# Kernel tuning notes

Measured on AMD Instinct MI355X. Metric: run time of the kernel, lower is better.

The kernel has to match this reference:

```python
import jax, jax.numpy as jnp
import numpy as np

C = 512
N_HEADS = 8
K_CH = C // N_HEADS          # 64
ROPE_D = int(K_CH * 0.5)     # 32, only first half of head dim is rotated
ROPE_BASE = 10000


def apply_rope(x):
    # x: [b, h, t, k_ch]; rotate first ROPE_D features, pass the rest through.
    t = x.shape[2]
    d = ROPE_D
    theta = 1.0 / (ROPE_BASE ** (jnp.arange(0, d, 2, dtype=jnp.float32) / d))  # [d/2]
    idx_theta = jnp.arange(t, dtype=jnp.float32)[:, None] * theta[None, :]     # [t, d/2]
    angles = jnp.concatenate([idx_theta, idx_theta], axis=-1)                  # [t, d]
    cos = jnp.cos(angles)[None, None, :, :].astype(x.dtype)
    sin = jnp.sin(angles)[None, None, :, :].astype(x.dtype)
    x_rope, x_pass = x[..., :d], x[..., d:]
    d2 = d // 2
    neg_half = jnp.concatenate([-x_rope[..., d2:], x_rope[..., :d2]], axis=-1)
    x_rope = x_rope * cos + neg_half * sin
    return jnp.concatenate([x_rope, x_pass], axis=-1)


def setup_inputs() -> dict:
    key = jax.random.key(0)
    ks = jax.random.split(key, 9)
    B, T = 16, 1024
    scale = 1.0 / np.sqrt(C)
    return {
        "x": jax.random.normal(ks[0], (B, C, T), dtype=jnp.float32),
        "Wq": jax.random.normal(ks[1], (C, C), dtype=jnp.float32) * scale,
        "bq": jax.random.normal(ks[2], (C,), dtype=jnp.float32) * 0.01,
        "Wk": jax.random.normal(ks[3], (C, C), dtype=jnp.float32) * scale,
        "bk": jax.random.normal(ks[4], (C,), dtype=jnp.float32) * 0.01,
        "Wv": jax.random.normal(ks[5], (C, C), dtype=jnp.float32) * scale,
        "bv": jax.random.normal(ks[6], (C,), dtype=jnp.float32) * 0.01,
        "Wo": jax.random.normal(ks[7], (C, C), dtype=jnp.float32) * scale,
        "bo": jax.random.normal(ks[8], (C,), dtype=jnp.float32) * 0.01,
    }


def reference(x, Wq, bq, Wk, bk, Wv, bv, Wo, bo):
    b, c, t = x.shape
    # 1x1 conv == channel matmul: [o,c] x [b,c,t] -> [b,o,t]
    q = jnp.einsum('oc,bct->bot', Wq, x) + bq[None, :, None]
    k = jnp.einsum('oc,bct->bot', Wk, x) + bk[None, :, None]
    v = jnp.einsum('oc,bct->bot', Wv, x) + bv[None, :, None]

    def to_heads(z):  # [b, c, t] -> [b, h, t, k_ch]
        return z.reshape(b, N_HEADS, K_CH, t).transpose(0, 1, 3, 2)

    q = apply_rope(to_heads(q))
    k = apply_rope(to_heads(k))
    v = to_heads(v)

    # scaled dot product attention (scale = 1/sqrt(head_dim))
    scores = jnp.einsum('bhqd,bhkd->bhqk', q, k) / np.sqrt(K_CH).astype(np.float32)
    attn = jax.nn.softmax(scores, axis=-1)
    out = jnp.einsum('bhqk,bhkd->bhqd', attn, v)  # [b, h, t, k_ch]

    out = out.transpose(0, 1, 3, 2).reshape(b, c, t)  # [b, c, t]
    return jnp.einsum('oc,bct->bot', Wo, out) + bo[None, :, None]
```

## Files before the change

### kernel.cpp

```cpp
#include <hip/hip_runtime.h>
#include <cmath>

#define B_  16
#define T_  1024
#define C_  512
#define NH_ 8
#define HD_ 64

#define AS1 __attribute__((address_space(1)))
#define AS3 __attribute__((address_space(3)))

#define FENCE_VM()   asm volatile("s_waitcnt vmcnt(0)" ::: "memory")
#define FENCE_LGKM() asm volatile("s_waitcnt lgkmcnt(0)" ::: "memory")

typedef __bf16 bf16_t;
typedef __bf16 bf16x8 __attribute__((ext_vector_type(8)));
typedef __bf16 bf16x4 __attribute__((ext_vector_type(4)));
typedef short  shortx8 __attribute__((ext_vector_type(8)));
typedef short  shortx4 __attribute__((ext_vector_type(4)));
typedef float  floatx4 __attribute__((ext_vector_type(4)));
typedef float  float4v __attribute__((ext_vector_type(4)));

__device__ inline float fast_exp2(float x) {
#if __has_builtin(__builtin_amdgcn_exp2f)
  return __builtin_amdgcn_exp2f(x);
#else
  float r; asm("v_exp_f32 %0, %1" : "=v"(r) : "v"(x)); return r;
#endif
}
__device__ inline float hw_sin_rev(float rev) {
  float r; asm("v_sin_f32 %0, %1" : "=v"(r) : "v"(rev)); return r;
}
__device__ inline float hw_cos_rev(float rev) {
  float r; asm("v_cos_f32 %0, %1" : "=v"(r) : "v"(rev)); return r;
}

template <typename V8>
__device__ inline auto mfma_impl(V8 a, V8 b, floatx4 c, int)
    -> decltype(__builtin_amdgcn_mfma_f32_16x16x32_bf16(a, b, c, 0, 0, 0)) {
  return __builtin_amdgcn_mfma_f32_16x16x32_bf16(a, b, c, 0, 0, 0);
}
template <typename V8>
__device__ inline floatx4 mfma_impl(V8 a, V8 b, floatx4 c, long) {
  return __builtin_amdgcn_mfma_f32_16x16x32_bf16(
      __builtin_bit_cast(shortx8, a), __builtin_bit_cast(shortx8, b), c, 0, 0, 0);
}
__device__ inline floatx4 mfma_bf16(bf16x8 a, bf16x8 b, floatx4 c) {
  return mfma_impl(a, b, c, 0);
}

__device__ inline floatx4 mfma16_bf16(bf16x4 a, bf16x4 b, floatx4 c) {
#if __has_builtin(__builtin_amdgcn_mfma_f32_16x16x16bf16_1k)
  return __builtin_amdgcn_mfma_f32_16x16x16bf16_1k(
      __builtin_bit_cast(shortx4, a), __builtin_bit_cast(shortx4, b), c, 0, 0, 0);
#else
  floatx4 d;
  asm("v_mfma_f32_16x16x16_bf16 %0, %1, %2, %3"
      : "=v"(d) : "v"(a), "v"(b), "0"(c));
  return d;
#endif
}

__global__ void prep(const float* __restrict__ x, bf16_t* __restrict__ xt,
                     const float* __restrict__ w0, const float* __restrict__ w1,
                     const float* __restrict__ w2, const float* __restrict__ w3,
                     bf16_t* __restrict__ d0, bf16_t* __restrict__ d1,
                     bf16_t* __restrict__ d2, bf16_t* __restrict__ d3) {
  const int tx = threadIdx.x, ty = threadIdx.y;
  if (blockIdx.z < 16) {
    __shared__ float tile[32][33];
    const int b = blockIdx.z;
    const int t0 = blockIdx.x * 32, c0 = blockIdx.y * 32;
    for (int i = ty; i < 32; i += 8)
      tile[i][tx] = x[((size_t)b * C_ + c0 + i) * T_ + t0 + tx];
    __syncthreads();
    for (int i = ty; i < 32; i += 8)
      xt[((size_t)b * T_ + t0 + i) * C_ + c0 + tx] = (bf16_t)tile[tx][i];
  } else {
    const float* s[4] = {w0, w1, w2, w3};
    bf16_t* d[4] = {d0, d1, d2, d3};
    const int tid = ty * 32 + tx;
    const int idx = (blockIdx.y * 32 + blockIdx.x) * 256 + tid;
    const int e0 = idx * 8;
    const int which = e0 >> 18;
    const int off = e0 & 262143;
    const float4v f0 = *(const float4v*)(s[which] + off);
    const float4v f1 = *(const float4v*)(s[which] + off + 4);
    bf16x8 o;
#pragma unroll
    for (int e = 0; e < 4; e++) { o[e] = (bf16_t)f0[e]; o[4 + e] = (bf16_t)f1[e]; }
    *(bf16x8*)(d[which] + off) = o;
  }
}

__global__ __launch_bounds__(256) void qkv_gemm(
    const bf16_t* __restrict__ Wq, const bf16_t* __restrict__ Wk, const bf16_t* __restrict__ Wv,
    const float* __restrict__ bq, const float* __restrict__ bk, const float* __restrict__ bv,
    const bf16_t* __restrict__ xt,
    bf16_t* __restrict__ qo, bf16_t* __restrict__ ko, bf16_t* __restrict__ vo) {
  const int which = blockIdx.z % 3;
  const int b = blockIdx.z / 3;
  const bf16_t* W = which == 0 ? Wq : (which == 1 ? Wk : Wv);
  const float* bias = which == 0 ? bq : (which == 1 ? bk : bv);
  const int wave = threadIdx.x >> 6, lane = threadIdx.x & 63;
  const int col = lane & 15, quad = lane >> 4;
  const int MbB = blockIdx.y * 128, NbB = blockIdx.x * 128;
  const int Mw = (wave >> 1) * 64, Nw = (wave & 1) * 64;
  const bf16_t* xb = xt + (size_t)b * T_ * C_;

  __shared__ bf16_t As[3][128 * 32];
  __shared__ bf16_t Bs[3][128 * 32];

  auto stageKV = [&](int i) {
    const int k0 = i * 32, buf = i % 3;
#pragma unroll
    for (int c = 0; c < 2; c++) {
      const int j = wave * 128 + c * 64 + lane;
      __builtin_amdgcn_global_load_lds(
          (const AS1 void*)(W + (MbB + (j >> 2)) * C_ + k0 + (j & 3) * 8),
          (AS3 void*)((char*)&As[buf][0] + wave * 2048 + c * 1024), 16, 0, 0);
    }
#pragma unroll
    for (int c = 0; c < 2; c++) {
      const int j = wave * 128 + c * 64 + lane;
      __builtin_amdgcn_global_load_lds(
          (const AS1 void*)(xb + (NbB + (j >> 2)) * C_ + k0 + (j & 3) * 8),
          (AS3 void*)((char*)&Bs[buf][0] + wave * 2048 + c * 1024), 16, 0, 0);
    }
  };

  floatx4 acc[4][4] = {};
  stageKV(0);
  stageKV(1);
  asm volatile("s_waitcnt vmcnt(4)\ns_barrier" ::: "memory");
  for (int i = 0; i < 16; i++) {
    if (i + 2 < 16) stageKV(i + 2);
    const bf16_t* a = &As[i % 3][0];
    const bf16_t* bb = &Bs[i % 3][0];
    bf16x8 af[4], bfr[4];
#pragma unroll
    for (int mi = 0; mi < 4; mi++)
      af[mi] = *(const bf16x8*)(a + (Mw + mi * 16 + col) * 32 + quad * 8);
#pragma unroll
    for (int ni = 0; ni < 4; ni++)
      bfr[ni] = *(const bf16x8*)(bb + (Nw + ni * 16 + col) * 32 + quad * 8);
#pragma unroll
    for (int mi = 0; mi < 4; mi++)
#pragma unroll
      for (int ni = 0; ni < 4; ni++)
        acc[mi][ni] = mfma_bf16(af[mi], bfr[ni], acc[mi][ni]);
    if (i < 14) {
      asm volatile("s_waitcnt vmcnt(4)\ns_barrier" ::: "memory");
    } else if (i == 14) {
      asm volatile("s_waitcnt vmcnt(0)\ns_barrier" ::: "memory");
    }
  }

  const int Mb = MbB + Mw, Nb = NbB + Nw;
#pragma unroll
  for (int mi = 0; mi < 4; mi++)
#pragma unroll
    for (int r = 0; r < 4; r++) {
      const float bval = bias[Mb + mi * 16 + quad * 4 + r];
#pragma unroll
      for (int ni = 0; ni < 4; ni++) acc[mi][ni][r] += bval;
    }

  const int h = Mb >> 6;
  if (which < 2) {
#pragma unroll
    for (int ni = 0; ni < 4; ni++) {
      const int t = Nb + ni * 16 + col;
#pragma unroll
      for (int r = 0; r < 4; r++) {
        const int dd = quad * 4 + r;
        const float theta_rev =
            fast_exp2(-(float)dd * 0.83048202372184059f - 2.6514961294723187f);
        float rev = (float)t * theta_rev;
        rev = rev - floorf(rev);
        const float sn = hw_sin_rev(rev), cs = hw_cos_rev(rev);
        const float a0 = acc[0][ni][r], a1 = acc[1][ni][r];
        acc[0][ni][r] = a0 * cs - a1 * sn;
        acc[1][ni][r] = a1 * cs + a0 * sn;
      }
    }
    bf16_t* out = which == 0 ? qo : ko;
#pragma unroll
    for (int mi = 0; mi < 4; mi++) {
      const int d0 = mi * 16 + quad * 4;
#pragma unroll
      for (int ni = 0; ni < 4; ni++) {
        const int t = Nb + ni * 16 + col;
        bf16x4 pk;
#pragma unroll
        for (int r = 0; r < 4; r++) pk[r] = (bf16_t)acc[mi][ni][r];
        *(bf16x4*)(out + ((size_t)(b * NH_ + h) * T_ + t) * HD_ + d0) = pk;
      }
    }
  } else {
#pragma unroll
    for (int mi = 0; mi < 4; mi++)
#pragma unroll
      for (int ni = 0; ni < 4; ni++) {
        const int t = Nb + ni * 16 + col;
#pragma unroll
        for (int r = 0; r < 4; r++) {
          const int d = mi * 16 + quad * 4 + r;
          vo[((size_t)(b * NH_ + h) * HD_ + d) * T_ + t] = (bf16_t)acc[mi][ni][r];
        }
      }
  }
}

__global__ __launch_bounds__(512, 4) void attn_kernel(
    const bf16_t* __restrict__ qb, const bf16_t* __restrict__ kb,
    const bf16_t* __restrict__ vtb, bf16_t* __restrict__ ob) {
  const int id = blockIdx.x;
  const int bh = id & 127;
  const int qt = id >> 7;
  const int tid = threadIdx.x;
  const int wave = tid >> 6, lane = tid & 63;
  const int col = lane & 15, quad = lane >> 4;
  const int tq0 = qt * 256 + wave * 32;

  const bf16_t* Q = qb + (size_t)bh * T_ * HD_;
  const bf16_t* K = kb + (size_t)bh * T_ * HD_;
  const bf16_t* VT = vtb + (size_t)bh * HD_ * T_;

  __shared__ bf16_t kvs[3][2][4096];

  auto stage = [&](const char* gRowBase, int rowStrideB, bf16_t* dst) {
    const int r = tid >> 3, ck = tid & 7;
    const char* src = gRowBase + r * rowStrideB + ((ck ^ (r & 7)) << 4);
    __builtin_amdgcn_global_load_lds(
        (const AS1 void*)src,
        (AS3 void*)((char*)dst + wave * 1024), 16, 0, 0);
  };
  auto stageKV = [&](int tk0, int buf) {
    stage((const char*)(K + (size_t)tk0 * HD_), HD_ * 2, &kvs[buf][0][0]);
    stage((const char*)VT + (size_t)tk0 * 2, T_ * 2, &kvs[buf][1][0]);
  };
  auto frag = [&](const bf16_t* base, int R, int cg) -> bf16x8 {
    return *(const bf16x8*)(base + R * 64 + ((cg ^ (R & 7)) << 3));
  };

  floatx4 oacc[2][4] = {};
  floatx4 lacc4[2] = {};
  const float CEXP = 0.18033688011112042f;

  stageKV(0, 0);
  stageKV(64, 1);
  bf16x8 qf[2][2];
#pragma unroll
  for (int g = 0; g < 2; g++)
#pragma unroll
    for (int kk = 0; kk < 2; kk++) {
      bf16x8 raw = *(const bf16x8*)(Q + (tq0 + g * 16 + col) * HD_ + kk * 32 + quad * 8);
#pragma unroll
      for (int e = 0; e < 8; e++) qf[g][kk][e] = (bf16_t)((float)raw[e] * CEXP);
    }
  FENCE_VM();
  __syncthreads();

  for (int it = 0; it < 16; it++) {
    const int buf = it % 3;
    if (it + 2 < 16) stageKV((it + 2) * 64, (it + 2) % 3);
    const bf16_t* kt = &kvs[buf][0][0];
    const bf16_t* vt = &kvs[buf][1][0];

    floatx4 s[2][4] = {};
#pragma unroll
    for (int ni = 0; ni < 4; ni++)
#pragma unroll
      for (int kk = 0; kk < 2; kk++) {
        const bf16x8 kf = frag(kt, ni * 16 + col, kk * 4 + quad);
        s[0][ni] = mfma_bf16(kf, qf[0][kk], s[0][ni]);
        s[1][ni] = mfma_bf16(kf, qf[1][kk], s[1][ni]);
      }

    bf16x4 p4[2][4];
#pragma unroll
    for (int g = 0; g < 2; g++)
#pragma unroll
      for (int ni = 0; ni < 4; ni++)
#pragma unroll
        for (int r = 0; r < 4; r++) {
          const float pv = fast_exp2(s[g][ni][r]);
          lacc4[g][r] += pv;
          p4[g][ni][r] = (bf16_t)pv;
        }

#pragma unroll
    for (int nd = 0; nd < 4; nd++) {
      const int R = nd * 16 + col;
      bf16x4 v4[4];
#pragma unroll
      for (int ni = 0; ni < 4; ni++) {
        const int c8 = ni * 2 + (quad >> 1);
        v4[ni] = *(const bf16x4*)(vt + R * 64 + ((c8 ^ (R & 7)) << 3) + (quad & 1) * 4);
      }
#pragma unroll
      for (int ni = 0; ni < 4; ni++) {
        oacc[0][nd] = mfma16_bf16(p4[0][ni], v4[ni], oacc[0][nd]);
        oacc[1][nd] = mfma16_bf16(p4[1][ni], v4[ni], oacc[1][nd]);
      }
    }

    if (it < 14) {
      asm volatile("s_waitcnt vmcnt(2)\ns_barrier" ::: "memory");
    } else if (it == 14) {
      asm volatile("s_waitcnt vmcnt(0)\ns_barrier" ::: "memory");
    }
  }

  float lrow[2];
#pragma unroll
  for (int g = 0; g < 2; g++) {
    lrow[g] = lacc4[g][0] + lacc4[g][1] + lacc4[g][2] + lacc4[g][3];
    lrow[g] += __shfl_xor(lrow[g], 16, 64);
    lrow[g] += __shfl_xor(lrow[g], 32, 64);
  }
  float linv[2][4];
#pragma unroll
  for (int g = 0; g < 2; g++)
#pragma unroll
    for (int r = 0; r < 4; r++)
      linv[g][r] = 1.0f / __shfl(lrow[g], quad * 4 + r, 64);
#pragma unroll
  for (int g = 0; g < 2; g++)
#pragma unroll
    for (int nd = 0; nd < 4; nd++)
#pragma unroll
      for (int r = 0; r < 4; r++) {
        const float v = oacc[g][nd][r] * linv[g][r];
        ob[((size_t)bh * T_ + tq0 + g * 16 + quad * 4 + r) * HD_ + nd * 16 + col] = (bf16_t)v;
      }
}

__global__ __launch_bounds__(256) void out_gemm(
    const bf16_t* __restrict__ W, const float* __restrict__ bias,
    const bf16_t* __restrict__ ao, float* __restrict__ y) {
  const int b = blockIdx.z;
  const int wave = threadIdx.x >> 6, lane = threadIdx.x & 63;
  const int col = lane & 15, quad = lane >> 4;
  const int MbB = blockIdx.y * 128, NbB = blockIdx.x * 128;
  const int Mw = (wave >> 1) * 64, Nw = (wave & 1) * 64;
  const bf16_t* ab = ao + (size_t)b * NH_ * T_ * HD_;

  __shared__ bf16_t As[3][128 * 32];
  __shared__ bf16_t Bs[3][128 * 32];

  auto stageKV = [&](int i) {
    const int k0 = i * 32, buf = i % 3;
#pragma unroll
    for (int c = 0; c < 2; c++) {
      const int j = wave * 128 + c * 64 + lane;
      __builtin_amdgcn_global_load_lds(
          (const AS1 void*)(W + (MbB + (j >> 2)) * C_ + k0 + (j & 3) * 8),
          (AS3 void*)((char*)&As[buf][0] + wave * 2048 + c * 1024), 16, 0, 0);
    }
#pragma unroll
    for (int c = 0; c < 2; c++) {
      const int j = wave * 128 + c * 64 + lane;
      const int kg = k0 + (j & 3) * 8;
      __builtin_amdgcn_global_load_lds(
          (const AS1 void*)(ab + ((size_t)(kg >> 6) * T_ + NbB + (j >> 2)) * HD_ + (kg & 63)),
          (AS3 void*)((char*)&Bs[buf][0] + wave * 2048 + c * 1024), 16, 0, 0);
    }
  };

  floatx4 acc[4][4] = {};
  stageKV(0);
  stageKV(1);
  asm volatile("s_waitcnt vmcnt(4)\ns_barrier" ::: "memory");
  for (int i = 0; i < 16; i++) {
    if (i + 2 < 16) stageKV(i + 2);
    const bf16_t* a = &As[i % 3][0];
    const bf16_t* bb = &Bs[i % 3][0];
    bf16x8 af[4], bfr[4];
#pragma unroll
    for (int mi = 0; mi < 4; mi++)
      af[mi] = *(const bf16x8*)(a + (Mw + mi * 16 + col) * 32 + quad * 8);
#pragma unroll
    for (int ni = 0; ni < 4; ni++)
      bfr[ni] = *(const bf16x8*)(bb + (Nw + ni * 16 + col) * 32 + quad * 8);
#pragma unroll
    for (int mi = 0; mi < 4; mi++)
#pragma unroll
      for (int ni = 0; ni < 4; ni++)
        acc[mi][ni] = mfma_bf16(af[mi], bfr[ni], acc[mi][ni]);
    if (i < 14) {
      asm volatile("s_waitcnt vmcnt(4)\ns_barrier" ::: "memory");
    } else if (i == 14) {
      asm volatile("s_waitcnt vmcnt(0)\ns_barrier" ::: "memory");
    }
  }

  const int Mb = MbB + Mw, Nb = NbB + Nw;
#pragma unroll
  for (int mi = 0; mi < 4; mi++)
#pragma unroll
    for (int r = 0; r < 4; r++) {
      const int o = Mb + mi * 16 + quad * 4 + r;
      const float bval = bias[o];
#pragma unroll
      for (int ni = 0; ni < 4; ni++) {
        const int t = Nb + ni * 16 + col;
        y[((size_t)b * C_ + o) * T_ + t] = acc[mi][ni][r] + bval;
      }
    }
}

extern "C" void kernel_launch(void* const* d_in, const int* in_sizes, int n_in,
                              void* d_out, int out_size, void* d_ws, size_t ws_size,
                              hipStream_t stream) {
  const float* x  = (const float*)d_in[0];
  const float* Wq = (const float*)d_in[1];
  const float* bq = (const float*)d_in[2];
  const float* Wk = (const float*)d_in[3];
  const float* bk = (const float*)d_in[4];
  const float* Wv = (const float*)d_in[5];
  const float* bv = (const float*)d_in[6];
  const float* Wo = (const float*)d_in[7];
  const float* bo = (const float*)d_in[8];
  float* y = (float*)d_out;

  char* ws = (char*)d_ws;
  const size_t WB = (size_t)C_ * C_ * 2;
  const size_t XB = (size_t)B_ * T_ * C_ * 2;
  bf16_t* wqb = (bf16_t*)(ws + 0 * WB);
  bf16_t* wkb = (bf16_t*)(ws + 1 * WB);
  bf16_t* wvb = (bf16_t*)(ws + 2 * WB);
  bf16_t* wob = (bf16_t*)(ws + 3 * WB);
  bf16_t* xt  = (bf16_t*)(ws + 4 * WB);
  bf16_t* qb_ = (bf16_t*)(ws + 4 * WB + 1 * XB);
  bf16_t* kb_ = (bf16_t*)(ws + 4 * WB + 2 * XB);
  bf16_t* vtb = (bf16_t*)(ws + 4 * WB + 3 * XB);
  bf16_t* aob = xt;

  prep<<<dim3(T_ / 32, C_ / 32, B_ + 1), dim3(32, 8), 0, stream>>>(
      x, xt, Wq, Wk, Wv, Wo, wqb, wkb, wvb, wob);
  qkv_gemm<<<dim3(T_ / 128, C_ / 128, B_ * 3), dim3(256), 0, stream>>>(
      wqb, wkb, wvb, bq, bk, bv, xt, qb_, kb_, vtb);
  attn_kernel<<<dim3((T_ / 256) * B_ * NH_), dim3(512), 0, stream>>>(qb_, kb_, vtb, aob);
  out_gemm<<<dim3(T_ / 128, C_ / 128, B_), dim3(256), 0, stream>>>(wob, bo, aob, y);
}
```

Baseline: 203.4 us.

## Vectorize x transpose in prep and use double-buffered qkv GEMM staging

```diff
diff --git a/kernel.cpp b/kernel.cpp
--- a/kernel.cpp
+++ b/kernel.cpp
@@ -67,20 +67,24 @@
                      bf16_t* __restrict__ d0, bf16_t* __restrict__ d1,
                      bf16_t* __restrict__ d2, bf16_t* __restrict__ d3) {
   const int tx = threadIdx.x, ty = threadIdx.y;
+  const int id = ty * 32 + tx;
   if (blockIdx.z < 16) {
-    __shared__ float tile[32][33];
+    __shared__ float tile[32][36];
     const int b = blockIdx.z;
     const int t0 = blockIdx.x * 32, c0 = blockIdx.y * 32;
-    for (int i = ty; i < 32; i += 8)
-      tile[i][tx] = x[((size_t)b * C_ + c0 + i) * T_ + t0 + tx];
+    const int cl = id >> 3, t4 = id & 7;
+    const float4v v = *(const float4v*)(x + ((size_t)b * C_ + c0 + cl) * T_ + t0 + t4 * 4);
+    *(float4v*)&tile[cl][t4 * 4] = v;
     __syncthreads();
-    for (int i = ty; i < 32; i += 8)
-      xt[((size_t)b * T_ + t0 + i) * C_ + c0 + tx] = (bf16_t)tile[tx][i];
+    const int tl = id >> 3, c4 = (id & 7) * 4;
+    bf16x4 pk;
+#pragma unroll
+    for (int j = 0; j < 4; j++) pk[j] = (bf16_t)tile[c4 + j][tl];
+    *(bf16x4*)(xt + ((size_t)b * T_ + t0 + tl) * C_ + c0 + c4) = pk;
   } else {
     const float* s[4] = {w0, w1, w2, w3};
     bf16_t* d[4] = {d0, d1, d2, d3};
-    const int tid = ty * 32 + tx;
-    const int idx = (blockIdx.y * 32 + blockIdx.x) * 256 + tid;
+    const int idx = (blockIdx.y * 32 + blockIdx.x) * 256 + id;
     const int e0 = idx * 8;
     const int which = e0 >> 18;
     const int off = e0 & 262143;
@@ -108,11 +112,11 @@
   const int Mw = (wave >> 1) * 64, Nw = (wave & 1) * 64;
   const bf16_t* xb = xt + (size_t)b * T_ * C_;
 
-  __shared__ bf16_t As[3][128 * 32];
-  __shared__ bf16_t Bs[3][128 * 32];
+  __shared__ bf16_t As[2][128 * 32];
+  __shared__ bf16_t Bs[2][128 * 32];
 
   auto stageKV = [&](int i) {
-    const int k0 = i * 32, buf = i % 3;
+    const int k0 = i * 32, buf = i & 1;
 #pragma unroll
     for (int c = 0; c < 2; c++) {
       const int j = wave * 128 + c * 64 + lane;
@@ -131,12 +135,12 @@
 
   floatx4 acc[4][4] = {};
   stageKV(0);
-  stageKV(1);
-  asm volatile("s_waitcnt vmcnt(4)\ns_barrier" ::: "memory");
+  FENCE_VM();
+  __syncthreads();
   for (int i = 0; i < 16; i++) {
-    if (i + 2 < 16) stageKV(i + 2);
-    const bf16_t* a = &As[i % 3][0];
-    const bf16_t* bb = &Bs[i % 3][0];
+    if (i + 1 < 16) stageKV(i + 1);
+    const bf16_t* a = &As[i & 1][0];
+    const bf16_t* bb = &Bs[i & 1][0];
     bf16x8 af[4], bfr[4];
 #pragma unroll
     for (int mi = 0; mi < 4; mi++)
@@ -149,10 +153,9 @@
 #pragma unroll
       for (int ni = 0; ni < 4; ni++)
         acc[mi][ni] = mfma_bf16(af[mi], bfr[ni], acc[mi][ni]);
-    if (i < 14) {
-      asm volatile("s_waitcnt vmcnt(4)\ns_barrier" ::: "memory");
-    } else if (i == 14) {
-      asm volatile("s_waitcnt vmcnt(0)\ns_barrier" ::: "memory");
+    if (i + 1 < 16) {
+      FENCE_VM();
+      __syncthreads();
     }
   }
 
```

Measured after the change: 202.4 us. About the same (-0.5%).
